# Kernel optimization log

Measured on AMD Instinct MI355X. Metric: run time of the kernel, lower is better.

## Reference

```python
import jax, jax.numpy as jnp
import numpy as np

N = 6144
IN_F = 512
OUT_F = 64
NHEADS = 8
ALPHA = 0.2  # leaky_relu negative slope
NEG_BIG = -1e10


def setup_inputs() -> dict:
    key = jax.random.key(0)
    k1, k2, k3, k4, k5 = jax.random.split(key, 5)
    x = jax.random.normal(k1, (N, IN_F), dtype=jnp.float32)
    adj = (jax.random.uniform(k2, (N, N)) < 0.01).astype(jnp.float32)
    adj = jnp.maximum(adj, jnp.eye(N, dtype=jnp.float32))
    weight = jax.random.normal(k3, (IN_F, NHEADS * OUT_F), dtype=jnp.float32) * 0.05
    linear_i = jax.random.normal(k4, (1, NHEADS, OUT_F), dtype=jnp.float32) * 0.05
    linear_j = jax.random.normal(k5, (1, NHEADS, OUT_F), dtype=jnp.float32) * 0.05
    return {"x": x, "adj": adj, "weight": weight, "linear_i": linear_i, "linear_j": linear_j}


def reference(x, adj, weight, linear_i, linear_j):
    # dropout p=0.0 (inference) -> identity
    wh = (x @ weight).reshape(-1, NHEADS, OUT_F)          # [N, H, F]
    awh_i = jnp.sum(wh * linear_i, axis=2)[:, None, :]    # [N, 1, H]
    awh_j = jnp.sum(wh * linear_j, axis=2)[None, :, :]    # [1, N, H]
    mask = (NEG_BIG * (1.0 - adj))[:, :, None]            # [N, N, 1]
    e = jax.nn.leaky_relu(awh_i + awh_j, negative_slope=ALPHA) + mask  # [N, N, H]
    a = jax.nn.softmax(e, axis=1)                          # softmax over source nodes j
    out = jnp.einsum('ijh,jhf->ihf', a, wh)               # [N, H, F]
    return out.reshape(out.shape[0], -1)                  # concat heads -> [N, H*F]
```

## Files before the change

### kernel.cpp

```cpp
#include <hip/hip_runtime.h>
#include <math.h>

#define N_NODES 6144
#define IN_FEAT 512
#define OUTW    512
#define NH      8
#define ALPHA   0.2f
#define CAP     128
#define GEMM_BLKS 768
#define CSR_BLKS  1536

typedef __attribute__((ext_vector_type(8))) short short8;
typedef __attribute__((ext_vector_type(4))) float f32x4;

__device__ __forceinline__ unsigned short f2bf(float f) {
    unsigned int u = __float_as_uint(f);
    u = (u + 0x7fffu + ((u >> 16) & 1u)) >> 16;
    return (unsigned short)u;
}
__device__ __forceinline__ float bf2f(unsigned short b) {
    return __uint_as_float(((unsigned int)b) << 16);
}

__global__ __launch_bounds__(256) void conv_w(const float* __restrict__ W,
                                              unsigned short* __restrict__ WThi,
                                              unsigned short* __restrict__ WTlo) {
    int n  = blockIdx.x * 8 + (threadIdx.x >> 5);
    int k0 = (threadIdx.x & 31) * 16;
    union { unsigned short u[16]; uint4 q[2]; } th, tl;
#pragma unroll
    for (int kk = 0; kk < 16; ++kk) {
        float v = W[(size_t)(k0 + kk) * OUTW + n];
        unsigned short hi = f2bf(v);
        th.u[kk] = hi;
        tl.u[kk] = f2bf(v - bf2f(hi));
    }
    uint4* ph = (uint4*)(WThi + (size_t)n * IN_FEAT + k0);
    uint4* pl = (uint4*)(WTlo + (size_t)n * IN_FEAT + k0);
    ph[0] = th.q[0]; ph[1] = th.q[1];
    pl[0] = tl.q[0]; pl[1] = tl.q[1];
}

__global__ __launch_bounds__(256) void gemm_csr(const float* __restrict__ X,
                                                const unsigned short* __restrict__ BThi,
                                                const unsigned short* __restrict__ BTlo,
                                                const float* __restrict__ LI,
                                                const float* __restrict__ LJ,
                                                const float* __restrict__ ADJ,
                                                unsigned short* __restrict__ WHB,
                                                float* __restrict__ AI,
                                                float* __restrict__ AJ,
                                                int* __restrict__ NBR,
                                                int* __restrict__ CNT) {
    __shared__ unsigned short As[64][40];
    __shared__ unsigned short Bh[64][40];
    __shared__ unsigned short Bl[64][40];
    __shared__ float s_ap[64][2], s_jp[64][2];
    const int tid = threadIdx.x;
    const int wave = tid >> 6, lane = tid & 63;

    if (blockIdx.x >= GEMM_BLKS) {
        const int row = (blockIdx.x - GEMM_BLKS) * 4 + wave;
        const f32x4* r4 = (const f32x4*)(ADJ + (size_t)row * N_NODES);
        int* dst = NBR + (size_t)row * CAP;
        const unsigned long long lt = (1ULL << lane) - 1;
        int base = 0;
#pragma unroll
        for (int q = 0; q < 24; ++q) {
            f32x4 v = __builtin_nontemporal_load(r4 + q * 64 + lane);
            int j = (q * 64 + lane) * 4;
#pragma unroll
            for (int c = 0; c < 4; ++c) {
                bool pred = v[c] > 0.5f;
                unsigned long long m = __ballot(pred);
                if (pred) {
                    int p = base + __popcll(m & lt);
                    if (p < CAP) dst[p] = j + c;
                }
                base += __popcll(m);
            }
        }
        if (lane == 0) CNT[row] = min(base, CAP);
        return;
    }

    const int bn = (blockIdx.x & 7) * 64, bm = (blockIdx.x >> 3) * 64;
    const int head = blockIdx.x & 7;
    const int wm0 = (wave & 1) * 32, wn0 = (wave >> 1) * 32;
    const int lm = lane & 15, lg = lane >> 4;
    const int ar = tid >> 2, akq = (tid & 3) * 8;
    f32x4 acc[2][2] = {};
    for (int k0 = 0; k0 < IN_FEAT; k0 += 32) {
        const float* ap = X + (size_t)(bm + ar) * IN_FEAT + k0 + akq;
        float4 f0 = *(const float4*)ap;
        float4 f1 = *(const float4*)(ap + 4);
        union { unsigned short u[8]; uint4 q; } ah;
        ah.u[0] = f2bf(f0.x); ah.u[1] = f2bf(f0.y);
        ah.u[2] = f2bf(f0.z); ah.u[3] = f2bf(f0.w);
        ah.u[4] = f2bf(f1.x); ah.u[5] = f2bf(f1.y);
        ah.u[6] = f2bf(f1.z); ah.u[7] = f2bf(f1.w);
        *(uint4*)&As[ar][akq] = ah.q;
        *(uint4*)&Bh[ar][akq] = *(const uint4*)(BThi + (size_t)(bn + ar) * IN_FEAT + k0 + akq);
        *(uint4*)&Bl[ar][akq] = *(const uint4*)(BTlo + (size_t)(bn + ar) * IN_FEAT + k0 + akq);
        __syncthreads();
        short8 a0  = *(const short8*)&As[wm0 + lm][lg * 8];
        short8 a1  = *(const short8*)&As[wm0 + 16 + lm][lg * 8];
        short8 bh0 = *(const short8*)&Bh[wn0 + lm][lg * 8];
        short8 bh1 = *(const short8*)&Bh[wn0 + 16 + lm][lg * 8];
        short8 bl0 = *(const short8*)&Bl[wn0 + lm][lg * 8];
        short8 bl1 = *(const short8*)&Bl[wn0 + 16 + lm][lg * 8];
        acc[0][0] = __builtin_amdgcn_mfma_f32_16x16x32_bf16(a0, bh0, acc[0][0], 0, 0, 0);
        acc[0][0] = __builtin_amdgcn_mfma_f32_16x16x32_bf16(a0, bl0, acc[0][0], 0, 0, 0);
        acc[0][1] = __builtin_amdgcn_mfma_f32_16x16x32_bf16(a0, bh1, acc[0][1], 0, 0, 0);
        acc[0][1] = __builtin_amdgcn_mfma_f32_16x16x32_bf16(a0, bl1, acc[0][1], 0, 0, 0);
        acc[1][0] = __builtin_amdgcn_mfma_f32_16x16x32_bf16(a1, bh0, acc[1][0], 0, 0, 0);
        acc[1][0] = __builtin_amdgcn_mfma_f32_16x16x32_bf16(a1, bl0, acc[1][0], 0, 0, 0);
        acc[1][1] = __builtin_amdgcn_mfma_f32_16x16x32_bf16(a1, bh1, acc[1][1], 0, 0, 0);
        acc[1][1] = __builtin_amdgcn_mfma_f32_16x16x32_bf16(a1, bl1, acc[1][1], 0, 0, 0);
        __syncthreads();
    }
#pragma unroll
    for (int fm = 0; fm < 2; ++fm)
#pragma unroll
        for (int fn = 0; fn < 2; ++fn)
#pragma unroll
            for (int r = 0; r < 4; ++r) {
                int row = bm + wm0 + fm * 16 + lg * 4 + r;
                int col = bn + wn0 + fn * 16 + lm;
                WHB[(size_t)row * OUTW + col] = f2bf(acc[fm][fn][r]);
            }
    float liv0 = LI[bn + wn0 + lm], liv1 = LI[bn + wn0 + 16 + lm];
    float ljv0 = LJ[bn + wn0 + lm], ljv1 = LJ[bn + wn0 + 16 + lm];
#pragma unroll
    for (int fm = 0; fm < 2; ++fm)
#pragma unroll
        for (int r = 0; r < 4; ++r) {
            float pa = acc[fm][0][r] * liv0 + acc[fm][1][r] * liv1;
            float pj = acc[fm][0][r] * ljv0 + acc[fm][1][r] * ljv1;
#pragma unroll
            for (int off = 1; off < 16; off <<= 1) {
                pa += __shfl_xor(pa, off);
                pj += __shfl_xor(pj, off);
            }
            if (lm == 0) {
                int row = wm0 + fm * 16 + lg * 4 + r;
                s_ap[row][wave >> 1] = pa;
                s_jp[row][wave >> 1] = pj;
            }
        }
    __syncthreads();
    if (tid < 64) {
        AI[(size_t)(bm + tid) * NH + head] = s_ap[tid][0] + s_ap[tid][1];
        AJ[(size_t)(bm + tid) * NH + head] = s_jp[tid][0] + s_jp[tid][1];
    }
}

__global__ __launch_bounds__(256) void gat_attn(const unsigned short* __restrict__ WHB,
                                                const float* __restrict__ AI,
                                                const float* __restrict__ AJ,
                                                const int* __restrict__ NBR,
                                                const int* __restrict__ CNT,
                                                float* __restrict__ OUT) {
    __shared__ int   s_nbr[CAP];
    __shared__ float s_p[CAP][5];
    __shared__ float s_comb[4][256];
    __shared__ float s_ai[4];
    __shared__ float s_red[4][4];
    __shared__ float s_m[4];
    __shared__ float s_d[4];

    const int i    = blockIdx.x;
    const int half = blockIdx.y;
    const int tid  = threadIdx.x;
    const int wid  = tid >> 6, lane = tid & 63;
    const int nc   = min(CNT[i], CAP);

    if (tid < 4) s_ai[tid] = AI[i * 8 + half * 4 + tid];
    if (tid < nc) s_nbr[tid] = NBR[(size_t)i * CAP + tid];
    __syncthreads();

    float mx[4] = {-1e30f, -1e30f, -1e30f, -1e30f};
    if (tid < nc) {
        int j = s_nbr[tid];
        float4 a0 = *(const float4*)(AJ + (size_t)j * 8 + half * 4);
        float z[4] = {a0.x, a0.y, a0.z, a0.w};
#pragma unroll
        for (int h = 0; h < 4; ++h) {
            float zz = s_ai[h] + z[h];
            float s  = zz > 0.f ? zz : ALPHA * zz;
            s_p[tid][h] = s;
            mx[h] = fmaxf(mx[h], s);
        }
    }
#pragma unroll
    for (int off = 32; off > 0; off >>= 1)
#pragma unroll
        for (int h = 0; h < 4; ++h) mx[h] = fmaxf(mx[h], __shfl_down(mx[h], off));
    if (lane == 0)
#pragma unroll
        for (int h = 0; h < 4; ++h) s_red[wid][h] = mx[h];
    __syncthreads();
    if (tid < 4)
        s_m[tid] = fmaxf(fmaxf(s_red[0][tid], s_red[1][tid]),
                         fmaxf(s_red[2][tid], s_red[3][tid]));
    __syncthreads();

    float sm[4] = {0.f, 0.f, 0.f, 0.f};
    if (tid < nc) {
#pragma unroll
        for (int h = 0; h < 4; ++h) {
            float p = __expf(s_p[tid][h] - s_m[h]);
            s_p[tid][h] = p;
            sm[h] += p;
        }
    }
#pragma unroll
    for (int off = 32; off > 0; off >>= 1)
#pragma unroll
        for (int h = 0; h < 4; ++h) sm[h] += __shfl_down(sm[h], off);
    if (lane == 0)
#pragma unroll
        for (int h = 0; h < 4; ++h) s_red[wid][h] = sm[h];
    __syncthreads();
    if (tid < 4)
        s_d[tid] = s_red[0][tid] + s_red[1][tid] + s_red[2][tid] + s_red[3][tid];
    __syncthreads();

    const int hd = lane >> 4;
    const unsigned short* wbase = WHB + half * 256 + lane * 4;
    float a4[4] = {};
    uint2 p0 = {}, p1 = {};
    if (wid < nc)     p0 = *(const uint2*)(wbase + (size_t)s_nbr[wid] * OUTW);
    if (wid + 4 < nc) p1 = *(const uint2*)(wbase + (size_t)s_nbr[wid + 4] * OUTW);
    for (int k = wid; k < nc; k += 4) {
        uint2 curw = p0;
        p0 = p1;
        if (k + 8 < nc) p1 = *(const uint2*)(wbase + (size_t)s_nbr[k + 8] * OUTW);
        float p = s_p[k][hd];
        a4[0] += p * __uint_as_float(curw.x << 16);
        a4[1] += p * __uint_as_float(curw.x & 0xFFFF0000u);
        a4[2] += p * __uint_as_float(curw.y << 16);
        a4[3] += p * __uint_as_float(curw.y & 0xFFFF0000u);
    }
#pragma unroll
    for (int q = 0; q < 4; ++q) s_comb[wid][lane * 4 + q] = a4[q];
    __syncthreads();
    if (tid < 64) {
        int c0 = tid * 4;
        int hh = tid >> 4;
        float4 v0 = *(const float4*)&s_comb[0][c0];
        float4 v1 = *(const float4*)&s_comb[1][c0];
        float4 v2 = *(const float4*)&s_comb[2][c0];
        float4 v3 = *(const float4*)&s_comb[3][c0];
        float inv = 1.0f / s_d[hh];
        f32x4 res;
        res.x = (v0.x + v1.x + v2.x + v3.x) * inv;
        res.y = (v0.y + v1.y + v2.y + v3.y) * inv;
        res.z = (v0.z + v1.z + v2.z + v3.z) * inv;
        res.w = (v0.w + v1.w + v2.w + v3.w) * inv;
        __builtin_nontemporal_store(res, (f32x4*)(OUT + (size_t)i * OUTW + half * 256 + c0));
    }
}

extern "C" void kernel_launch(void* const* d_in, const int* in_sizes, int n_in,
                              void* d_out, int out_size, void* d_ws, size_t ws_size,
                              hipStream_t stream) {
    const float* x   = (const float*)d_in[0];
    const float* adj = (const float*)d_in[1];
    const float* w   = (const float*)d_in[2];
    const float* li  = (const float*)d_in[3];
    const float* lj  = (const float*)d_in[4];
    float* out = (float*)d_out;

    unsigned short* whb = (unsigned short*)d_ws;
    float* ai = (float*)(whb + (size_t)N_NODES * OUTW);
    float* aj = ai + (size_t)N_NODES * NH;
    unsigned short* wthi = (unsigned short*)(aj + (size_t)N_NODES * NH);
    unsigned short* wtlo = wthi + (size_t)OUTW * IN_FEAT;
    int* nbr = (int*)(wtlo + (size_t)OUTW * IN_FEAT);
    int* cnt = nbr + (size_t)N_NODES * CAP;

    conv_w<<<OUTW / 8, 256, 0, stream>>>(w, wthi, wtlo);
    gemm_csr<<<GEMM_BLKS + CSR_BLKS, 256, 0, stream>>>(
        x, wthi, wtlo, li, lj, adj, whb, ai, aj, nbr, cnt);
    gat_attn<<<dim3(N_NODES, 2), 256, 0, stream>>>(whb, ai, aj, nbr, cnt, out);
}
```

Measured before the change: 113.4 us.

## Drop bf16 split-weight GEMM, pre-convert X, interleave CSR blocks, widen gather loads

Removes the hi/lo bf16 split of the weight so the GEMM issues half as many MFMAs and stages one B tile instead of two. X is converted to bf16 once in a separate prep kernel rather than inside the GEMM loop. GEMM and adjacency-scan blocks are interleaved one-to-two so both kinds of work are spread across the grid. The attention gather uses 16-byte loads with two neighbours per wave and deeper prefetch. The price is lower weight precision and an extra round trip of X through global memory.

```diff
diff --git a/kernel.cpp b/kernel.cpp
--- a/kernel.cpp
+++ b/kernel.cpp
@@ -7,8 +7,7 @@
 #define NH      8
 #define ALPHA   0.2f
 #define CAP     128
-#define GEMM_BLKS 768
-#define CSR_BLKS  1536
+#define TOTAL_BLKS 2304
 
 typedef __attribute__((ext_vector_type(8))) short short8;
 typedef __attribute__((ext_vector_type(4))) float f32x4;
@@ -18,32 +17,34 @@
     u = (u + 0x7fffu + ((u >> 16) & 1u)) >> 16;
     return (unsigned short)u;
 }
-__device__ __forceinline__ float bf2f(unsigned short b) {
-    return __uint_as_float(((unsigned int)b) << 16);
-}
-
-__global__ __launch_bounds__(256) void conv_w(const float* __restrict__ W,
-                                              unsigned short* __restrict__ WThi,
-                                              unsigned short* __restrict__ WTlo) {
-    int n  = blockIdx.x * 8 + (threadIdx.x >> 5);
-    int k0 = (threadIdx.x & 31) * 16;
-    union { unsigned short u[16]; uint4 q[2]; } th, tl;
-#pragma unroll
-    for (int kk = 0; kk < 16; ++kk) {
-        float v = W[(size_t)(k0 + kk) * OUTW + n];
-        unsigned short hi = f2bf(v);
-        th.u[kk] = hi;
-        tl.u[kk] = f2bf(v - bf2f(hi));
-    }
-    uint4* ph = (uint4*)(WThi + (size_t)n * IN_FEAT + k0);
-    uint4* pl = (uint4*)(WTlo + (size_t)n * IN_FEAT + k0);
-    ph[0] = th.q[0]; ph[1] = th.q[1];
-    pl[0] = tl.q[0]; pl[1] = tl.q[1];
-}
-
-__global__ __launch_bounds__(256) void gemm_csr(const float* __restrict__ X,
-                                                const unsigned short* __restrict__ BThi,
-                                                const unsigned short* __restrict__ BTlo,
+
+__global__ __launch_bounds__(256) void prep(const float* __restrict__ W,
+                                            const float* __restrict__ X,
+                                            unsigned short* __restrict__ WT,
+                                            unsigned short* __restrict__ XB) {
+    const int tid = threadIdx.x;
+    if (blockIdx.x < 64) {
+        int n  = blockIdx.x * 8 + (tid >> 5);
+        int k0 = (tid & 31) * 16;
+        union { unsigned short u[16]; uint4 q[2]; } th;
+#pragma unroll
+        for (int kk = 0; kk < 16; ++kk)
+            th.u[kk] = f2bf(W[(size_t)(k0 + kk) * OUTW + n]);
+        uint4* ph = (uint4*)(WT + (size_t)n * IN_FEAT + k0);
+        ph[0] = th.q[0]; ph[1] = th.q[1];
+        return;
+    }
+    const size_t base = (size_t)(blockIdx.x - 64) * 2048 + tid * 8;
+    float4 f0 = *(const float4*)(X + base);
+    float4 f1 = *(const float4*)(X + base + 4);
+    union { unsigned short u[8]; uint4 q; } r;
+    r.u[0] = f2bf(f0.x); r.u[1] = f2bf(f0.y); r.u[2] = f2bf(f0.z); r.u[3] = f2bf(f0.w);
+    r.u[4] = f2bf(f1.x); r.u[5] = f2bf(f1.y); r.u[6] = f2bf(f1.z); r.u[7] = f2bf(f1.w);
+    *(uint4*)(XB + base) = r.q;
+}
+
+__global__ __launch_bounds__(256) void gemm_csr(const unsigned short* __restrict__ XB,
+                                                const unsigned short* __restrict__ BT,
                                                 const float* __restrict__ LI,
                                                 const float* __restrict__ LJ,
                                                 const float* __restrict__ ADJ,
@@ -54,13 +55,14 @@
                                                 int* __restrict__ CNT) {
     __shared__ unsigned short As[64][40];
     __shared__ unsigned short Bh[64][40];
-    __shared__ unsigned short Bl[64][40];
     __shared__ float s_ap[64][2], s_jp[64][2];
     const int tid = threadIdx.x;
     const int wave = tid >> 6, lane = tid & 63;
-
-    if (blockIdx.x >= GEMM_BLKS) {
-        const int row = (blockIdx.x - GEMM_BLKS) * 4 + wave;
+    const int bid = blockIdx.x;
+    const int g = bid / 3, r3 = bid - g * 3;
+
+    if (r3 != 0) {
+        const int row = (g * 2 + (r3 - 1)) * 4 + wave;
         const f32x4* r4 = (const f32x4*)(ADJ + (size_t)row * N_NODES);
         int* dst = NBR + (size_t)row * CAP;
         const unsigned long long lt = (1ULL << lane) - 1;
@@ -84,39 +86,24 @@
         return;
     }
 
-    const int bn = (blockIdx.x & 7) * 64, bm = (blockIdx.x >> 3) * 64;
-    const int head = blockIdx.x & 7;
+    const int bn = (g & 7) * 64, bm = (g >> 3) * 64;
+    const int head = g & 7;
     const int wm0 = (wave & 1) * 32, wn0 = (wave >> 1) * 32;
     const int lm = lane & 15, lg = lane >> 4;
     const int ar = tid >> 2, akq = (tid & 3) * 8;
     f32x4 acc[2][2] = {};
     for (int k0 = 0; k0 < IN_FEAT; k0 += 32) {
-        const float* ap = X + (size_t)(bm + ar) * IN_FEAT + k0 + akq;
-        float4 f0 = *(const float4*)ap;
-        float4 f1 = *(const float4*)(ap + 4);
-        union { unsigned short u[8]; uint4 q; } ah;
-        ah.u[0] = f2bf(f0.x); ah.u[1] = f2bf(f0.y);
-        ah.u[2] = f2bf(f0.z); ah.u[3] = f2bf(f0.w);
-        ah.u[4] = f2bf(f1.x); ah.u[5] = f2bf(f1.y);
-        ah.u[6] = f2bf(f1.z); ah.u[7] = f2bf(f1.w);
-        *(uint4*)&As[ar][akq] = ah.q;
-        *(uint4*)&Bh[ar][akq] = *(const uint4*)(BThi + (size_t)(bn + ar) * IN_FEAT + k0 + akq);
-        *(uint4*)&Bl[ar][akq] = *(const uint4*)(BTlo + (size_t)(bn + ar) * IN_FEAT + k0 + akq);
+        *(uint4*)&As[ar][akq] = *(const uint4*)(XB + (size_t)(bm + ar) * IN_FEAT + k0 + akq);
+        *(uint4*)&Bh[ar][akq] = *(const uint4*)(BT + (size_t)(bn + ar) * IN_FEAT + k0 + akq);
         __syncthreads();
         short8 a0  = *(const short8*)&As[wm0 + lm][lg * 8];
         short8 a1  = *(const short8*)&As[wm0 + 16 + lm][lg * 8];
         short8 bh0 = *(const short8*)&Bh[wn0 + lm][lg * 8];
         short8 bh1 = *(const short8*)&Bh[wn0 + 16 + lm][lg * 8];
-        short8 bl0 = *(const short8*)&Bl[wn0 + lm][lg * 8];
-        short8 bl1 = *(const short8*)&Bl[wn0 + 16 + lm][lg * 8];
         acc[0][0] = __builtin_amdgcn_mfma_f32_16x16x32_bf16(a0, bh0, acc[0][0], 0, 0, 0);
-        acc[0][0] = __builtin_amdgcn_mfma_f32_16x16x32_bf16(a0, bl0, acc[0][0], 0, 0, 0);
         acc[0][1] = __builtin_amdgcn_mfma_f32_16x16x32_bf16(a0, bh1, acc[0][1], 0, 0, 0);
-        acc[0][1] = __builtin_amdgcn_mfma_f32_16x16x32_bf16(a0, bl1, acc[0][1], 0, 0, 0);
         acc[1][0] = __builtin_amdgcn_mfma_f32_16x16x32_bf16(a1, bh0, acc[1][0], 0, 0, 0);
-        acc[1][0] = __builtin_amdgcn_mfma_f32_16x16x32_bf16(a1, bl0, acc[1][0], 0, 0, 0);
         acc[1][1] = __builtin_amdgcn_mfma_f32_16x16x32_bf16(a1, bh1, acc[1][1], 0, 0, 0);
-        acc[1][1] = __builtin_amdgcn_mfma_f32_16x16x32_bf16(a1, bl1, acc[1][1], 0, 0, 0);
         __syncthreads();
     }
 #pragma unroll
@@ -163,7 +150,7 @@
                                                 float* __restrict__ OUT) {
     __shared__ int   s_nbr[CAP];
     __shared__ float s_p[CAP][5];
-    __shared__ float s_comb[4][256];
+    __shared__ float s_comb[4][2][256];
     __shared__ float s_ai[4];
     __shared__ float s_red[4][4];
     __shared__ float s_m[4];
@@ -226,39 +213,52 @@
         s_d[tid] = s_red[0][tid] + s_red[1][tid] + s_red[2][tid] + s_red[3][tid];
     __syncthreads();
 
-    const int hd = lane >> 4;
-    const unsigned short* wbase = WHB + half * 256 + lane * 4;
-    float a4[4] = {};
-    uint2 p0 = {}, p1 = {};
-    if (wid < nc)     p0 = *(const uint2*)(wbase + (size_t)s_nbr[wid] * OUTW);
-    if (wid + 4 < nc) p1 = *(const uint2*)(wbase + (size_t)s_nbr[wid + 4] * OUTW);
-    for (int k = wid; k < nc; k += 4) {
-        uint2 curw = p0;
-        p0 = p1;
-        if (k + 8 < nc) p1 = *(const uint2*)(wbase + (size_t)s_nbr[k + 8] * OUTW);
+    const int sub = lane >> 5;
+    const int c32 = lane & 31;
+    const int hd  = c32 >> 3;
+    const unsigned short* wbase = WHB + (size_t)half * 256 + c32 * 8;
+    float a8[8] = {};
+    uint4 p0 = {}, p1 = {}, p2 = {};
+    int k = wid * 2 + sub;
+    if (k < nc)      p0 = *(const uint4*)(wbase + (size_t)s_nbr[k] * OUTW);
+    if (k + 8 < nc)  p1 = *(const uint4*)(wbase + (size_t)s_nbr[k + 8] * OUTW);
+    if (k + 16 < nc) p2 = *(const uint4*)(wbase + (size_t)s_nbr[k + 16] * OUTW);
+    for (; k < nc; k += 8) {
+        uint4 cur = p0;
+        p0 = p1; p1 = p2;
+        if (k + 24 < nc) p2 = *(const uint4*)(wbase + (size_t)s_nbr[k + 24] * OUTW);
         float p = s_p[k][hd];
-        a4[0] += p * __uint_as_float(curw.x << 16);
-        a4[1] += p * __uint_as_float(curw.x & 0xFFFF0000u);
-        a4[2] += p * __uint_as_float(curw.y << 16);
-        a4[3] += p * __uint_as_float(curw.y & 0xFFFF0000u);
-    }
-#pragma unroll
-    for (int q = 0; q < 4; ++q) s_comb[wid][lane * 4 + q] = a4[q];
+        unsigned int uu[4] = {cur.x, cur.y, cur.z, cur.w};
+#pragma unroll
+        for (int q = 0; q < 4; ++q) {
+            float lo = __uint_as_float(uu[q] << 16);
+            float hi = __uint_as_float(uu[q] & 0xFFFF0000u);
+            a8[2 * q]     += p * lo;
+            a8[2 * q + 1] += p * hi;
+        }
+    }
+#pragma unroll
+    for (int q = 0; q < 8; ++q) s_comb[wid][sub][c32 * 8 + q] = a8[q];
     __syncthreads();
     if (tid < 64) {
         int c0 = tid * 4;
         int hh = tid >> 4;
-        float4 v0 = *(const float4*)&s_comb[0][c0];
-        float4 v1 = *(const float4*)&s_comb[1][c0];
-        float4 v2 = *(const float4*)&s_comb[2][c0];
-        float4 v3 = *(const float4*)&s_comb[3][c0];
+        float4 r0 = *(const float4*)&s_comb[0][0][c0];
+        float4 r1 = *(const float4*)&s_comb[0][1][c0];
+        float4 r2 = *(const float4*)&s_comb[1][0][c0];
+        float4 r3 = *(const float4*)&s_comb[1][1][c0];
+        float4 r4 = *(const float4*)&s_comb[2][0][c0];
+        float4 r5 = *(const float4*)&s_comb[2][1][c0];
+        float4 r6 = *(const float4*)&s_comb[3][0][c0];
+        float4 r7 = *(const float4*)&s_comb[3][1][c0];
         float inv = 1.0f / s_d[hh];
         f32x4 res;
-        res.x = (v0.x + v1.x + v2.x + v3.x) * inv;
-        res.y = (v0.y + v1.y + v2.y + v3.y) * inv;
-        res.z = (v0.z + v1.z + v2.z + v3.z) * inv;
-        res.w = (v0.w + v1.w + v2.w + v3.w) * inv;
-        __builtin_nontemporal_store(res, (f32x4*)(OUT + (size_t)i * OUTW + half * 256 + c0));
+        res.x = (r0.x + r1.x + r2.x + r3.x + r4.x + r5.x + r6.x + r7.x) * inv;
+        res.y = (r0.y + r1.y + r2.y + r3.y + r4.y + r5.y + r6.y + r7.y) * inv;
+        res.z = (r0.z + r1.z + r2.z + r3.z + r4.z + r5.z + r6.z + r7.z) * inv;
+        res.w = (r0.w + r1.w + r2.w + r3.w + r4.w + r5.w + r6.w + r7.w) * inv;
+        __builtin_nontemporal_store(res,
+            (f32x4*)(OUT + (size_t)i * OUTW + half * 256 + c0));
     }
 }
 
@@ -275,13 +275,13 @@
     unsigned short* whb = (unsigned short*)d_ws;
     float* ai = (float*)(whb + (size_t)N_NODES * OUTW);
     float* aj = ai + (size_t)N_NODES * NH;
-    unsigned short* wthi = (unsigned short*)(aj + (size_t)N_NODES * NH);
-    unsigned short* wtlo = wthi + (size_t)OUTW * IN_FEAT;
-    int* nbr = (int*)(wtlo + (size_t)OUTW * IN_FEAT);
+    unsigned short* wt = (unsigned short*)(aj + (size_t)N_NODES * NH);
+    unsigned short* xb = wt + (size_t)OUTW * IN_FEAT;
+    int* nbr = (int*)(xb + (size_t)N_NODES * IN_FEAT);
     int* cnt = nbr + (size_t)N_NODES * CAP;
 
-    conv_w<<<OUTW / 8, 256, 0, stream>>>(w, wthi, wtlo);
-    gemm_csr<<<GEMM_BLKS + CSR_BLKS, 256, 0, stream>>>(
-        x, wthi, wtlo, li, lj, adj, whb, ai, aj, nbr, cnt);
+    prep<<<64 + N_NODES / 4, 256, 0, stream>>>(w, x, wt, xb);
+    gemm_csr<<<TOTAL_BLKS, 256, 0, stream>>>(
+        xb, wt, li, lj, adj, whb, ai, aj, nbr, cnt);
     gat_attn<<<dim3(N_NODES, 2), 256, 0, stream>>>(whb, ai, aj, nbr, cnt, out);
 }
```

After: 105.9 us. 1.07x faster.
